# Kernel optimization log

Measured on AMD Instinct MI355X. Metric: run time of the kernel, lower is better.

The kernel has to match this reference:

```python
import jax, jax.numpy as jnp
import numpy as np

N_SRC0, N_DST0 = 200000, 50000
N_DST1 = 10000
D_IN, D_HID = 128, 128


def _sage_mean(h, src, dst, n_dst, W_self, b_self, W_neigh, b_neigh, act):
    # gather messages from src nodes, mean-aggregate per dst node
    msg = h[src]                                             # [E, D]
    agg = jax.ops.segment_sum(msg, dst, num_segments=n_dst)  # [n_dst, D]
    deg = jax.ops.segment_sum(jnp.ones(dst.shape, h.dtype), dst, num_segments=n_dst)
    h_neigh = agg / jnp.maximum(deg, 1.0)[:, None]
    # DGL block convention: dst nodes are the first n_dst src nodes
    rst = h[:n_dst] @ W_self + b_self + h_neigh @ W_neigh + b_neigh
    return jax.nn.relu(rst) if act else rst


def setup_inputs() -> dict:
    key = jax.random.key(0)
    ks = jax.random.split(key, 12)
    s = 1.0 / np.sqrt(D_HID)
    return {
        "features": jax.random.normal(ks[0], (N_SRC0, D_IN), jnp.float32),
        "src0": jax.random.randint(ks[1], (800000,), 0, N_SRC0),
        "dst0": jax.random.randint(ks[2], (800000,), 0, N_DST0),
        "src1": jax.random.randint(ks[3], (160000,), 0, N_DST0),
        "dst1": jax.random.randint(ks[4], (160000,), 0, N_DST1),
        "W_init": jax.random.uniform(ks[5], (D_IN, D_HID), jnp.float32, -s, s),
        "b_init": jax.random.uniform(ks[6], (D_HID,), jnp.float32, -s, s),
        "W_self": jax.random.uniform(ks[7], (D_HID, D_HID), jnp.float32, -s, s),
        "b_self": jax.random.uniform(ks[8], (D_HID,), jnp.float32, -s, s),
        "W_neigh": jax.random.uniform(ks[9], (D_HID, D_HID), jnp.float32, -s, s),
        "b_neigh": jax.random.uniform(ks[10], (D_HID,), jnp.float32, -s, s),
    }


def reference(features, src0, dst0, src1, dst1, W_init, b_init, W_self, b_self, W_neigh, b_neigh):
    # fc_init + activation
    h = jax.nn.relu(features @ W_init + b_init)              # [N_SRC0, D_HID]
    # block 0 (act_flag True), dropout p=0.0 is identity
    h = _sage_mean(h, src0, dst0, N_DST0, W_self, b_self, W_neigh, b_neigh, act=True)
    # block 1 (last block: act_flag False)
    h = _sage_mean(h, src1, dst1, N_DST1, W_self, b_self, W_neigh, b_neigh, act=False)
    return jnp.squeeze(h, axis=1) if h.shape[1] == 1 else h  # h.squeeze(1) no-op for D_HID>1
```

## Files before the change

### kernel.cpp

```cpp
#include <hip/hip_runtime.h>
#include <stdint.h>
#include <stddef.h>


#define DIM 128
constexpr int N_SRC0 = 200000;
constexpr int N_DST0 = 50000;
constexpr int N_DST1 = 10000;
constexpr int E0 = 800000;
constexpr int E1 = 160000;
constexpr int MAXDEG = 64;

typedef __attribute__((ext_vector_type(8))) short bf16x8;
typedef __attribute__((ext_vector_type(4))) float f32x4;

__device__ __forceinline__ uint16_t f2bf(float f) {
  union { float f; uint32_t u; } v; v.f = f;
  return (uint16_t)((v.u + 0x7FFFu + ((v.u >> 16) & 1u)) >> 16);
}
__device__ __forceinline__ float bf2f(uint16_t h) {
  union { uint32_t u; float f; } v; v.u = ((uint32_t)h) << 16;
  return v.f;
}

__global__ __launch_bounds__(512) void prep_w_kernel(
    const float* __restrict__ W0, const float* __restrict__ W1,
    const float* __restrict__ W2, uint16_t* __restrict__ Wf,
    int* __restrict__ cnt, int ncnt) {
  int gid = blockIdx.x * 512 + threadIdx.x;
  if (gid < 3 * 16384) {
    int m = gid >> 14, idx = gid & 16383;
    const float* W = m == 0 ? W0 : (m == 1 ? W1 : W2);
    int j = idx & 7, lane = (idx >> 3) & 63, nt = (idx >> 9) & 7, kc = idx >> 12;
    int k = kc * 32 + (lane >> 4) * 8 + j;
    int n = nt * 16 + (lane & 15);
    Wf[gid] = f2bf(W[k * DIM + n]);
  }
  int z = gid - 3 * 16384;
  if (z >= 0 && z < ncnt) cnt[z] = 0;
}

__global__ __launch_bounds__(256) void place_kernel(
    const int* __restrict__ src0, const int* __restrict__ dst0,
    const int* __restrict__ src1, const int* __restrict__ dst1,
    int* __restrict__ cnt0, int* __restrict__ cnt1,
    int* __restrict__ eslot0, int* __restrict__ eslot1) {
  int i = blockIdx.x * 256 + threadIdx.x;
  if (i < E0) {
    int d = dst0[i];
    int p = atomicAdd(&cnt0[d], 1);
    if (p < MAXDEG) eslot0[(size_t)d * MAXDEG + p] = src0[i];
  } else if (i - E0 < E1) {
    int j = i - E0;
    int d = dst1[j];
    int p = atomicAdd(&cnt1[d], 1);
    if (p < MAXDEG) eslot1[(size_t)d * MAXDEG + p] = src1[j];
  }
}

__global__ __launch_bounds__(256) void fc_init_kernel(
    const float* __restrict__ feat, const uint16_t* __restrict__ Wf,
    const float* __restrict__ bias, uint16_t* __restrict__ hout) {
  __shared__ uint16_t wl[16384];
  {
    const uint4* g = (const uint4*)Wf;
    uint4* s = (uint4*)wl;
    for (int i = threadIdx.x; i < 2048; i += 256) s[i] = g[i];
  }
  __syncthreads();

  int wave = (blockIdx.x * 256 + threadIdx.x) >> 6;
  int nwaves = (gridDim.x * 256) >> 6;
  int lane = threadIdx.x & 63;
  int q = lane >> 4, m16 = lane & 15;

  float bv[8];
#pragma unroll
  for (int nt = 0; nt < 8; nt++) bv[nt] = bias[nt * 16 + m16];

  const int nstrips = N_SRC0 / 16;
  int s = wave;
  float4 X[8];
  if (s < nstrips) {
    const float* ap = feat + (size_t)(s * 16 + m16) * DIM + q * 8;
#pragma unroll
    for (int kc = 0; kc < 4; kc++) {
      X[2 * kc]     = *(const float4*)(ap + kc * 32);
      X[2 * kc + 1] = *(const float4*)(ap + kc * 32 + 4);
    }
  }

  while (s < nstrips) {
    int sn = s + nwaves;
    float4 Y[8];
    if (sn < nstrips) {
      const float* ap = feat + (size_t)(sn * 16 + m16) * DIM + q * 8;
#pragma unroll
      for (int kc = 0; kc < 4; kc++) {
        Y[2 * kc]     = *(const float4*)(ap + kc * 32);
        Y[2 * kc + 1] = *(const float4*)(ap + kc * 32 + 4);
      }
    }

    f32x4 acc[8];
#pragma unroll
    for (int nt = 0; nt < 8; nt++) acc[nt] = (f32x4){0.f, 0.f, 0.f, 0.f};

#pragma unroll
    for (int kc = 0; kc < 4; kc++) {
      float xs[8] = {X[2 * kc].x, X[2 * kc].y, X[2 * kc].z, X[2 * kc].w,
                     X[2 * kc + 1].x, X[2 * kc + 1].y, X[2 * kc + 1].z, X[2 * kc + 1].w};
      bf16x8 a;
#pragma unroll
      for (int j = 0; j < 8; j++) a[j] = (short)f2bf(xs[j]);
#pragma unroll
      for (int nt = 0; nt < 8; nt++) {
        bf16x8 w = *(const bf16x8*)&wl[(size_t)((kc * 8 + nt) * 64 + lane) * 8];
        acc[nt] = __builtin_amdgcn_mfma_f32_16x16x32_bf16(a, w, acc[nt], 0, 0, 0);
      }
    }

    int m0 = s * 16;
#pragma unroll
    for (int nt = 0; nt < 8; nt++)
#pragma unroll
      for (int r = 0; r < 4; r++) {
        float v = fmaxf(acc[nt][r] + bv[nt], 0.f);
        hout[(size_t)(m0 + q * 4 + r) * DIM + nt * 16 + m16] = f2bf(v);
      }

#pragma unroll
    for (int i = 0; i < 8; i++) X[i] = Y[i];
    s = sn;
  }
}

__global__ __launch_bounds__(256) void agg_kernel(
    const int* __restrict__ eslot, const int* __restrict__ deg,
    const uint16_t* __restrict__ hsrc, uint16_t* __restrict__ hout, int n_dst) {
  int d = (blockIdx.x * 256 + threadIdx.x) >> 6;
  int lane = threadIdx.x & 63;
  if (d >= n_dst) return;
  const int* sl = eslot + (size_t)d * MAXDEG;
  int dg = deg[d];
  int dgc = dg < MAXDEG ? dg : MAXDEG;
  float a0 = 0.f, a1 = 0.f;
  int e = 0;
  for (; e + 4 <= dgc; e += 4) {
    int s0 = sl[e], s1 = sl[e + 1], s2 = sl[e + 2], s3 = sl[e + 3];
    uint32_t p0 = *(const uint32_t*)(hsrc + (size_t)s0 * DIM + lane * 2);
    uint32_t p1 = *(const uint32_t*)(hsrc + (size_t)s1 * DIM + lane * 2);
    uint32_t p2 = *(const uint32_t*)(hsrc + (size_t)s2 * DIM + lane * 2);
    uint32_t p3 = *(const uint32_t*)(hsrc + (size_t)s3 * DIM + lane * 2);
    a0 += bf2f((uint16_t)p0) + bf2f((uint16_t)p1) + bf2f((uint16_t)p2) + bf2f((uint16_t)p3);
    a1 += bf2f((uint16_t)(p0 >> 16)) + bf2f((uint16_t)(p1 >> 16)) +
          bf2f((uint16_t)(p2 >> 16)) + bf2f((uint16_t)(p3 >> 16));
  }
  for (; e < dgc; e++) {
    uint32_t p = *(const uint32_t*)(hsrc + (size_t)sl[e] * DIM + lane * 2);
    a0 += bf2f((uint16_t)p);
    a1 += bf2f((uint16_t)(p >> 16));
  }
  float inv = 1.f / fmaxf((float)dg, 1.f);
  uint32_t o = (uint32_t)f2bf(a0 * inv) | ((uint32_t)f2bf(a1 * inv) << 16);
  *(uint32_t*)(hout + (size_t)d * DIM + lane * 2) = o;
}

template <bool ACT, bool OUT_BF16>
__global__ __launch_bounds__(256) void sage_kernel(
    const uint16_t* __restrict__ hself, const uint16_t* __restrict__ hneigh,
    const uint16_t* __restrict__ WfS, const uint16_t* __restrict__ WfN,
    const float* __restrict__ bS, const float* __restrict__ bN,
    void* __restrict__ outp, int n_dst) {
  __shared__ uint16_t wS[16384];
  __shared__ uint16_t wN[16384];
  {
    const uint4* gS = (const uint4*)WfS;
    const uint4* gN = (const uint4*)WfN;
    uint4* sS = (uint4*)wS;
    uint4* sN = (uint4*)wN;
    for (int i = threadIdx.x; i < 2048; i += 256) { sS[i] = gS[i]; sN[i] = gN[i]; }
  }
  __syncthreads();

  int wave = (blockIdx.x * 256 + threadIdx.x) >> 6;
  int nwaves = (gridDim.x * 256) >> 6;
  int lane = threadIdx.x & 63;
  int q = lane >> 4, m16 = lane & 15;

  float bv[8];
#pragma unroll
  for (int nt = 0; nt < 8; nt++)
    bv[nt] = bS[nt * 16 + m16] + bN[nt * 16 + m16];

  const int nstrips = n_dst / 16;
  int s = wave;
  bf16x8 XS[4], XN[4];
  if (s < nstrips) {
    size_t ro = (size_t)(s * 16 + m16) * DIM + q * 8;
#pragma unroll
    for (int kc = 0; kc < 4; kc++) {
      XS[kc] = *(const bf16x8*)(hself + ro + kc * 32);
      XN[kc] = *(const bf16x8*)(hneigh + ro + kc * 32);
    }
  }

  while (s < nstrips) {
    int sn = s + nwaves;
    bf16x8 YS[4], YN[4];
    if (sn < nstrips) {
      size_t ro = (size_t)(sn * 16 + m16) * DIM + q * 8;
#pragma unroll
      for (int kc = 0; kc < 4; kc++) {
        YS[kc] = *(const bf16x8*)(hself + ro + kc * 32);
        YN[kc] = *(const bf16x8*)(hneigh + ro + kc * 32);
      }
    }

    f32x4 acc[8];
#pragma unroll
    for (int nt = 0; nt < 8; nt++) acc[nt] = (f32x4){0.f, 0.f, 0.f, 0.f};

#pragma unroll
    for (int kc = 0; kc < 4; kc++) {
#pragma unroll
      for (int nt = 0; nt < 8; nt++) {
        size_t fo = (size_t)((kc * 8 + nt) * 64 + lane) * 8;
        bf16x8 ws = *(const bf16x8*)&wS[fo];
        bf16x8 wn = *(const bf16x8*)&wN[fo];
        acc[nt] = __builtin_amdgcn_mfma_f32_16x16x32_bf16(XS[kc], ws, acc[nt], 0, 0, 0);
        acc[nt] = __builtin_amdgcn_mfma_f32_16x16x32_bf16(XN[kc], wn, acc[nt], 0, 0, 0);
      }
    }

    int m0 = s * 16;
#pragma unroll
    for (int nt = 0; nt < 8; nt++)
#pragma unroll
      for (int r = 0; r < 4; r++) {
        float v = acc[nt][r] + bv[nt];
        if (ACT) v = fmaxf(v, 0.f);
        size_t o = (size_t)(m0 + q * 4 + r) * DIM + nt * 16 + m16;
        if (OUT_BF16) ((uint16_t*)outp)[o] = f2bf(v);
        else          ((float*)outp)[o] = v;
      }

#pragma unroll
    for (int i = 0; i < 4; i++) { XS[i] = YS[i]; XN[i] = YN[i]; }
    s = sn;
  }
}

extern "C" void kernel_launch(void* const* d_in, const int* in_sizes, int n_in,
                              void* d_out, int out_size, void* d_ws, size_t ws_size,
                              hipStream_t stream) {
  const float* feat   = (const float*)d_in[0];
  const int* src0     = (const int*)d_in[1];
  const int* dst0     = (const int*)d_in[2];
  const int* src1     = (const int*)d_in[3];
  const int* dst1     = (const int*)d_in[4];
  const float* W_init = (const float*)d_in[5];
  const float* b_init = (const float*)d_in[6];
  const float* W_self = (const float*)d_in[7];
  const float* b_self = (const float*)d_in[8];
  const float* W_neigh= (const float*)d_in[9];
  const float* b_neigh= (const float*)d_in[10];

  char* ws = (char*)d_ws;
  uint16_t* h     = (uint16_t*)(ws + 0);
  uint16_t* h1    = (uint16_t*)(ws + 51200000);
  uint16_t* hn    = (uint16_t*)(ws + 64000000);
  int*      cnt0  = (int*)(ws + 76800000);
  int*      cnt1  = (int*)(ws + 77000000);
  int*      eslot0= (int*)(ws + 77040000);
  int*      eslot1= (int*)(ws + 89840000);
  uint16_t* WfI   = (uint16_t*)(ws + 92400000);
  uint16_t* WfS   = WfI + 16384;
  uint16_t* WfN   = WfS + 16384;

  prep_w_kernel<<<214, 512, 0, stream>>>(W_init, W_self, W_neigh, WfI, cnt0, 60000);
  place_kernel<<<(E0 + E1 + 255) / 256, 256, 0, stream>>>(
      src0, dst0, src1, dst1, cnt0, cnt1, eslot0, eslot1);

  fc_init_kernel<<<768, 256, 0, stream>>>(feat, WfI, b_init, h);

  agg_kernel<<<N_DST0 / 4, 256, 0, stream>>>(eslot0, cnt0, h, hn, N_DST0);
  sage_kernel<true, true><<<512, 256, 0, stream>>>(h, hn, WfS, WfN, b_self, b_neigh,
                                                   h1, N_DST0);

  agg_kernel<<<N_DST1 / 4, 256, 0, stream>>>(eslot1, cnt1, h1, hn, N_DST1);
  sage_kernel<false, false><<<160, 256, 0, stream>>>(h1, hn, WfS, WfN, b_self, b_neigh,
                                                     d_out, N_DST1);
}
```

Before: 313.5 us.

## Partition edge placement by destination range and stage fc_init tiles via async LDS loads

The edge placement kernel now reads indices as int4, and each block handles only destinations in one of eight partitions, so the atomics and slot writes for a given range come from a subset of blocks and should have better locality. The cost is that every partition rereads the full edge arrays. fc_init now double-buffers 32-row feature tiles into shared memory with global_load_lds, and the waves split the output columns between them. This is meant to overlap the feature loads with MFMA work, at the cost of more LDS use and a block-wide barrier on every tile.

```diff
diff --git a/kernel.cpp b/kernel.cpp
--- a/kernel.cpp
+++ b/kernel.cpp
@@ -45,16 +45,29 @@
     const int* __restrict__ src1, const int* __restrict__ dst1,
     int* __restrict__ cnt0, int* __restrict__ cnt1,
     int* __restrict__ eslot0, int* __restrict__ eslot1) {
-  int i = blockIdx.x * 256 + threadIdx.x;
-  if (i < E0) {
-    int d = dst0[i];
-    int p = atomicAdd(&cnt0[d], 1);
-    if (p < MAXDEG) eslot0[(size_t)d * MAXDEG + p] = src0[i];
-  } else if (i - E0 < E1) {
-    int j = i - E0;
-    int d = dst1[j];
-    int p = atomicAdd(&cnt1[d], 1);
-    if (p < MAXDEG) eslot1[(size_t)d * MAXDEG + p] = src1[j];
+  int part = blockIdx.x & 7;
+  int bpp  = gridDim.x >> 3;
+  int bidx = blockIdx.x >> 3;
+  const int4* s04 = (const int4*)src0;
+  const int4* d04 = (const int4*)dst0;
+  const int4* s14 = (const int4*)src1;
+  const int4* d14 = (const int4*)dst1;
+
+  int lo = part * (N_DST0 / 8), hi = lo + (N_DST0 / 8);
+  for (int i = bidx * 256 + threadIdx.x; i < E0 / 4; i += bpp * 256) {
+    int4 d = d04[i]; int4 s = s04[i];
+    if (d.x >= lo && d.x < hi) { int p = atomicAdd(&cnt0[d.x], 1); if (p < MAXDEG) eslot0[(size_t)d.x * MAXDEG + p] = s.x; }
+    if (d.y >= lo && d.y < hi) { int p = atomicAdd(&cnt0[d.y], 1); if (p < MAXDEG) eslot0[(size_t)d.y * MAXDEG + p] = s.y; }
+    if (d.z >= lo && d.z < hi) { int p = atomicAdd(&cnt0[d.z], 1); if (p < MAXDEG) eslot0[(size_t)d.z * MAXDEG + p] = s.z; }
+    if (d.w >= lo && d.w < hi) { int p = atomicAdd(&cnt0[d.w], 1); if (p < MAXDEG) eslot0[(size_t)d.w * MAXDEG + p] = s.w; }
+  }
+  int lo1 = part * (N_DST1 / 8), hi1 = lo1 + (N_DST1 / 8);
+  for (int i = bidx * 256 + threadIdx.x; i < E1 / 4; i += bpp * 256) {
+    int4 d = d14[i]; int4 s = s14[i];
+    if (d.x >= lo1 && d.x < hi1) { int p = atomicAdd(&cnt1[d.x], 1); if (p < MAXDEG) eslot1[(size_t)d.x * MAXDEG + p] = s.x; }
+    if (d.y >= lo1 && d.y < hi1) { int p = atomicAdd(&cnt1[d.y], 1); if (p < MAXDEG) eslot1[(size_t)d.y * MAXDEG + p] = s.y; }
+    if (d.z >= lo1 && d.z < hi1) { int p = atomicAdd(&cnt1[d.z], 1); if (p < MAXDEG) eslot1[(size_t)d.z * MAXDEG + p] = s.z; }
+    if (d.w >= lo1 && d.w < hi1) { int p = atomicAdd(&cnt1[d.w], 1); if (p < MAXDEG) eslot1[(size_t)d.w * MAXDEG + p] = s.w; }
   }
 }
 
@@ -62,76 +75,78 @@
     const float* __restrict__ feat, const uint16_t* __restrict__ Wf,
     const float* __restrict__ bias, uint16_t* __restrict__ hout) {
   __shared__ uint16_t wl[16384];
+  __shared__ __align__(16) float tile[2][4096];
   {
     const uint4* g = (const uint4*)Wf;
     uint4* s = (uint4*)wl;
     for (int i = threadIdx.x; i < 2048; i += 256) s[i] = g[i];
   }
+  const int tid = threadIdx.x;
+  const int w = tid >> 6, lane = tid & 63;
+  const int q = lane >> 4, m16 = lane & 15;
+  const int sl = w >> 1, nh = w & 1;
+
+  float bv[4];
+#pragma unroll
+  for (int j = 0; j < 4; j++) bv[j] = bias[(nh * 4 + j) * 16 + m16];
+
+  const int ntiles = N_SRC0 / 32;
+  const int stride = gridDim.x;
+
+  auto stage = [&](int t, int buf) {
+    const float* gbase = feat + (size_t)t * 4096 + w * 1024 + lane * 4;
+    float* lbase = &tile[buf][w * 1024];
+#pragma unroll
+    for (int i = 0; i < 4; i++) {
+      __builtin_amdgcn_global_load_lds(
+          (const __attribute__((address_space(1))) uint32_t*)(gbase + i * 256),
+          (__attribute__((address_space(3))) uint32_t*)(lbase + i * 256),
+          16, 0, 0);
+    }
+  };
+
+  int t = blockIdx.x;
+  int cur = 0;
+  if (t < ntiles) stage(t, 0);
   __syncthreads();
 
-  int wave = (blockIdx.x * 256 + threadIdx.x) >> 6;
-  int nwaves = (gridDim.x * 256) >> 6;
-  int lane = threadIdx.x & 63;
-  int q = lane >> 4, m16 = lane & 15;
-
-  float bv[8];
-#pragma unroll
-  for (int nt = 0; nt < 8; nt++) bv[nt] = bias[nt * 16 + m16];
-
-  const int nstrips = N_SRC0 / 16;
-  int s = wave;
-  float4 X[8];
-  if (s < nstrips) {
-    const float* ap = feat + (size_t)(s * 16 + m16) * DIM + q * 8;
+  while (t < ntiles) {
+    int tn = t + stride;
+    if (tn < ntiles) stage(tn, cur ^ 1);
+
+    f32x4 acc[4];
+#pragma unroll
+    for (int j = 0; j < 4; j++) acc[j] = (f32x4){0.f, 0.f, 0.f, 0.f};
+
+    const float* arow = &tile[cur][(sl * 16 + m16) * 128];
 #pragma unroll
     for (int kc = 0; kc < 4; kc++) {
-      X[2 * kc]     = *(const float4*)(ap + kc * 32);
-      X[2 * kc + 1] = *(const float4*)(ap + kc * 32 + 4);
-    }
-  }
-
-  while (s < nstrips) {
-    int sn = s + nwaves;
-    float4 Y[8];
-    if (sn < nstrips) {
-      const float* ap = feat + (size_t)(sn * 16 + m16) * DIM + q * 8;
-#pragma unroll
-      for (int kc = 0; kc < 4; kc++) {
-        Y[2 * kc]     = *(const float4*)(ap + kc * 32);
-        Y[2 * kc + 1] = *(const float4*)(ap + kc * 32 + 4);
-      }
-    }
-
-    f32x4 acc[8];
-#pragma unroll
-    for (int nt = 0; nt < 8; nt++) acc[nt] = (f32x4){0.f, 0.f, 0.f, 0.f};
-
-#pragma unroll
-    for (int kc = 0; kc < 4; kc++) {
-      float xs[8] = {X[2 * kc].x, X[2 * kc].y, X[2 * kc].z, X[2 * kc].w,
-                     X[2 * kc + 1].x, X[2 * kc + 1].y, X[2 * kc + 1].z, X[2 * kc + 1].w};
+      float4 x0 = *(const float4*)(arow + kc * 32 + q * 8);
+      float4 x1 = *(const float4*)(arow + kc * 32 + q * 8 + 4);
+      float xs[8] = {x0.x, x0.y, x0.z, x0.w, x1.x, x1.y, x1.z, x1.w};
       bf16x8 a;
 #pragma unroll
       for (int j = 0; j < 8; j++) a[j] = (short)f2bf(xs[j]);
 #pragma unroll
-      for (int nt = 0; nt < 8; nt++) {
-        bf16x8 w = *(const bf16x8*)&wl[(size_t)((kc * 8 + nt) * 64 + lane) * 8];
-        acc[nt] = __builtin_amdgcn_mfma_f32_16x16x32_bf16(a, w, acc[nt], 0, 0, 0);
-      }
-    }
-
-    int m0 = s * 16;
-#pragma unroll
-    for (int nt = 0; nt < 8; nt++)
+      for (int j = 0; j < 4; j++) {
+        int nt = nh * 4 + j;
+        bf16x8 wv = *(const bf16x8*)&wl[((kc * 8 + nt) * 64 + lane) * 8];
+        acc[j] = __builtin_amdgcn_mfma_f32_16x16x32_bf16(a, wv, acc[j], 0, 0, 0);
+      }
+    }
+
+    int rowb = t * 32 + sl * 16 + q * 4;
+#pragma unroll
+    for (int j = 0; j < 4; j++)
 #pragma unroll
       for (int r = 0; r < 4; r++) {
-        float v = fmaxf(acc[nt][r] + bv[nt], 0.f);
-        hout[(size_t)(m0 + q * 4 + r) * DIM + nt * 16 + m16] = f2bf(v);
-      }
-
-#pragma unroll
-    for (int i = 0; i < 8; i++) X[i] = Y[i];
-    s = sn;
+        float v = fmaxf(acc[j][r] + bv[j], 0.f);
+        hout[(size_t)(rowb + r) * DIM + (nh * 4 + j) * 16 + m16] = f2bf(v);
+      }
+
+    __syncthreads();
+    cur ^= 1;
+    t = tn;
   }
 }
 
@@ -279,10 +294,10 @@
   uint16_t* WfN   = WfS + 16384;
 
   prep_w_kernel<<<214, 512, 0, stream>>>(W_init, W_self, W_neigh, WfI, cnt0, 60000);
-  place_kernel<<<(E0 + E1 + 255) / 256, 256, 0, stream>>>(
-      src0, dst0, src1, dst1, cnt0, cnt1, eslot0, eslot1);
-
-  fc_init_kernel<<<768, 256, 0, stream>>>(feat, WfI, b_init, h);
+  place_kernel<<<1024, 256, 0, stream>>>(src0, dst0, src1, dst1,
+                                         cnt0, cnt1, eslot0, eslot1);
+
+  fc_init_kernel<<<512, 256, 0, stream>>>(feat, WfI, b_init, h);
 
   agg_kernel<<<N_DST0 / 4, 256, 0, stream>>>(eslot0, cnt0, h, hn, N_DST0);
   sage_kernel<true, true><<<512, 256, 0, stream>>>(h, hn, WfS, WfN, b_self, b_neigh,
```

Measured after the change: 306.1 us. -2.4%, faster.
